# Kernel optimization log

Hardware: AMD Instinct MI355X
Metric: run time of the kernel (lower is better)

## Reference

```python
import jax, jax.numpy as jnp
import numpy as np

HIDDEN = 32


def setup_inputs() -> dict:
    key = jax.random.key(0)
    ks = jax.random.split(key, 7)
    B, T = 16384, 1024
    s = 1.0 / np.sqrt(HIDDEN)  # torch RNNCell/Linear init scale (uniform bound)
    return {
        "x": jax.random.normal(ks[0], (B, T, 1), dtype=jnp.float32),
        "W_ih": jax.random.uniform(ks[1], (HIDDEN, 1), jnp.float32, -s, s),
        "W_hh": jax.random.uniform(ks[2], (HIDDEN, HIDDEN), jnp.float32, -s, s),
        "b_ih": jax.random.uniform(ks[3], (HIDDEN,), jnp.float32, -s, s),
        "b_hh": jax.random.uniform(ks[4], (HIDDEN,), jnp.float32, -s, s),
        "fc_w": jax.random.uniform(ks[5], (1, HIDDEN), jnp.float32, -s, s),
        "fc_b": jax.random.uniform(ks[6], (1,), jnp.float32, -s, s),
    }


def reference(x, W_ih, W_hh, b_ih, b_hh, fc_w, fc_b):
    # x: [B, T, 1]; vanilla tanh RNN over T, then linear head on final hidden.
    B, T, _ = x.shape
    # Precompute input projections for all timesteps: [T, B, H]
    xi = jnp.einsum("bti,hi->tbh", x, W_ih) + b_ih + b_hh
    h0 = jnp.zeros((B, HIDDEN), dtype=x.dtype)

    def step(h, xi_t):
        h = jnp.tanh(xi_t + h @ W_hh.T)
        return h, None

    h_final, _ = jax.lax.scan(step, h0, xi)
    return h_final @ fc_w.T + fc_b  # [B, 1]
```

## Files before the change

kernel.cpp:

```cpp
#include <hip/hip_runtime.h>

#define T_LEN 1024

typedef _Float16 f16x8 __attribute__((ext_vector_type(8)));
typedef __fp16   fp16x2 __attribute__((ext_vector_type(2)));
typedef float    f32x4 __attribute__((ext_vector_type(4)));

__global__ __launch_bounds__(64) void rnn_fused(
    const float* __restrict__ x,
    const float* __restrict__ W_ih,
    const float* __restrict__ W_hh,
    const float* __restrict__ b_ih,
    const float* __restrict__ b_hh,
    const float* __restrict__ fc_w,
    const float* __restrict__ fc_b,
    float* __restrict__ out)
{
    const int lane = threadIdx.x;
    const int n = lane & 15;
    const int q = lane >> 4;

    const float K = 2.88539008177792681472f;

    const int c0row = 8 * (n >> 2) + (n & 3);
    const int c1row = c0row + 4;
    f16x8 a0, a1;
#pragma unroll
    for (int j = 0; j < 8; ++j) {
        a0[j] = (_Float16)(-2.0f * K * W_hh[c0row * 32 + q * 8 + j]);
        a1[j] = (_Float16)(-2.0f * K * W_hh[c1row * 32 + q * 8 + j]);
    }

    float wih[8], bias[8];
#pragma unroll
    for (int i = 0; i < 8; ++i) {
        int c = 8 * q + i;
        float rs = 0.0f;
        for (int k = 0; k < 32; ++k) rs += W_hh[c * 32 + k];
        wih[i]  = K * W_ih[c];
        bias[i] = K * (b_ih[c] + b_hh[c] + rs);
    }

    const float* xrow = x + (size_t)(blockIdx.x * 16 + n) * T_LEN;
    float4 xa = *(const float4*)xrow;

    f16x8 hb;
#pragma unroll
    for (int i = 0; i < 8; ++i) hb[i] = (_Float16)0.5f;

    for (int t4 = 0; t4 < T_LEN / 4; ++t4) {
        const int nt4 = (t4 < T_LEN / 4 - 1) ? t4 + 1 : t4;
        float4 xn = *(const float4*)(xrow + (size_t)nt4 * 4);
#pragma unroll
        for (int p = 0; p < 4; ++p) {
            const float xt = (p == 0) ? xa.x : (p == 1) ? xa.y : (p == 2) ? xa.z : xa.w;
            f32x4 acc0, acc1;
#pragma unroll
            for (int i = 0; i < 4; ++i) {
                acc0[i] = fmaf(xt, wih[i],     bias[i]);
                acc1[i] = fmaf(xt, wih[4 + i], bias[4 + i]);
            }
            acc0 = __builtin_amdgcn_mfma_f32_16x16x32_f16(a0, hb, acc0, 0, 0, 0);
            acc1 = __builtin_amdgcn_mfma_f32_16x16x32_f16(a1, hb, acc1, 0, 0, 0);

            float e0 = __builtin_amdgcn_exp2f(acc0[0]);
            float e1 = __builtin_amdgcn_exp2f(acc0[1]);
            float e2 = __builtin_amdgcn_exp2f(acc0[2]);
            float e3 = __builtin_amdgcn_exp2f(acc0[3]);
            float e4 = __builtin_amdgcn_exp2f(acc1[0]);
            float e5 = __builtin_amdgcn_exp2f(acc1[1]);
            float e6 = __builtin_amdgcn_exp2f(acc1[2]);
            float e7 = __builtin_amdgcn_exp2f(acc1[3]);
            float r0 = __builtin_amdgcn_rcpf(e0 + 1.0f);
            float r1 = __builtin_amdgcn_rcpf(e1 + 1.0f);
            float r2 = __builtin_amdgcn_rcpf(e2 + 1.0f);
            float r3 = __builtin_amdgcn_rcpf(e3 + 1.0f);
            float r4 = __builtin_amdgcn_rcpf(e4 + 1.0f);
            float r5 = __builtin_amdgcn_rcpf(e5 + 1.0f);
            float r6 = __builtin_amdgcn_rcpf(e6 + 1.0f);
            float r7 = __builtin_amdgcn_rcpf(e7 + 1.0f);

            struct H4 { fp16x2 p[4]; } hh;
            hh.p[0] = __builtin_amdgcn_cvt_pkrtz(r0, r1);
            hh.p[1] = __builtin_amdgcn_cvt_pkrtz(r2, r3);
            hh.p[2] = __builtin_amdgcn_cvt_pkrtz(r4, r5);
            hh.p[3] = __builtin_amdgcn_cvt_pkrtz(r6, r7);
            hb = __builtin_bit_cast(f16x8, hh);
        }
        xa = xn;
    }

    float part = 0.0f;
#pragma unroll
    for (int i = 0; i < 8; ++i) {
        float h = fmaf(-2.0f, (float)hb[i], 1.0f);
        part = fmaf(h, fc_w[8 * q + i], part);
    }
    part += __shfl_xor(part, 16);
    part += __shfl_xor(part, 32);
    if (q == 0) out[blockIdx.x * 16 + n] = part + fc_b[0];
}

extern "C" void kernel_launch(void* const* d_in, const int* in_sizes, int n_in,
                              void* d_out, int out_size, void* d_ws, size_t ws_size,
                              hipStream_t stream) {
    const float* x    = (const float*)d_in[0];
    const float* W_ih = (const float*)d_in[1];
    const float* W_hh = (const float*)d_in[2];
    const float* b_ih = (const float*)d_in[3];
    const float* b_hh = (const float*)d_in[4];
    const float* fc_w = (const float*)d_in[5];
    const float* fc_b = (const float*)d_in[6];
    float* out = (float*)d_out;

    const int B = in_sizes[0] / T_LEN;
    rnn_fused<<<B / 16, 64, 0, stream>>>(x, W_ih, W_hh, b_ih, b_hh, fc_w, fc_b, out);
}
```

Before: 254.9 us.

## Split hidden units across two wavefronts exchanging state through shared memory

Each 16-sequence block now runs two wavefronts, each computing 16 of the 32 hidden units with a single MFMA per step instead of two. The new hidden halves are written to a double-buffered LDS tile and read back after a block barrier to form the next step's input. This shortens each wave's serial chain of MFMA and transcendental work. In exchange it adds an LDS round trip and a __syncthreads on every one of the 1024 timesteps, which sits on the critical recurrence path.

```diff
diff --git a/kernel.cpp b/kernel.cpp
--- a/kernel.cpp
+++ b/kernel.cpp
@@ -6,7 +6,7 @@
 typedef __fp16   fp16x2 __attribute__((ext_vector_type(2)));
 typedef float    f32x4 __attribute__((ext_vector_type(4)));
 
-__global__ __launch_bounds__(64) void rnn_fused(
+__global__ __launch_bounds__(128) void rnn_fused(
     const float* __restrict__ x,
     const float* __restrict__ W_ih,
     const float* __restrict__ W_hh,
@@ -16,25 +16,25 @@
     const float* __restrict__ fc_b,
     float* __restrict__ out)
 {
-    const int lane = threadIdx.x;
+    const int tid  = threadIdx.x;
+    const int w    = tid >> 6;
+    const int lane = tid & 63;
     const int n = lane & 15;
     const int q = lane >> 4;
 
     const float K = 2.88539008177792681472f;
 
-    const int c0row = 8 * (n >> 2) + (n & 3);
-    const int c1row = c0row + 4;
-    f16x8 a0, a1;
+    __shared__ __align__(16) _Float16 rbuf[2][16][40];
+
+    f16x8 a;
 #pragma unroll
-    for (int j = 0; j < 8; ++j) {
-        a0[j] = (_Float16)(-2.0f * K * W_hh[c0row * 32 + q * 8 + j]);
-        a1[j] = (_Float16)(-2.0f * K * W_hh[c1row * 32 + q * 8 + j]);
-    }
+    for (int j = 0; j < 8; ++j)
+        a[j] = (_Float16)(-2.0f * K * W_hh[(16 * w + n) * 32 + 8 * q + j]);
 
-    float wih[8], bias[8];
+    float wih[4], bias[4];
 #pragma unroll
-    for (int i = 0; i < 8; ++i) {
-        int c = 8 * q + i;
+    for (int i = 0; i < 4; ++i) {
+        int c = 16 * w + 4 * q + i;
         float rs = 0.0f;
         for (int k = 0; k < 32; ++k) rs += W_hh[c * 32 + k];
         wih[i]  = K * W_ih[c];
@@ -48,57 +48,56 @@
 #pragma unroll
     for (int i = 0; i < 8; ++i) hb[i] = (_Float16)0.5f;
 
+    _Float16* wrp = &rbuf[0][n][16 * w + 4 * q];
+    const _Float16* rdp = &rbuf[0][n][8 * q];
+    const int BUFSTRIDE = 16 * 40;
+
     for (int t4 = 0; t4 < T_LEN / 4; ++t4) {
         const int nt4 = (t4 < T_LEN / 4 - 1) ? t4 + 1 : t4;
         float4 xn = *(const float4*)(xrow + (size_t)nt4 * 4);
 #pragma unroll
-        for (int p = 0; p < 4; ++p) {
-            const float xt = (p == 0) ? xa.x : (p == 1) ? xa.y : (p == 2) ? xa.z : xa.w;
-            f32x4 acc0, acc1;
+        for (int pp = 0; pp < 4; ++pp) {
+            const float xt = (pp == 0) ? xa.x : (pp == 1) ? xa.y : (pp == 2) ? xa.z : xa.w;
+            f32x4 acc;
 #pragma unroll
-            for (int i = 0; i < 4; ++i) {
-                acc0[i] = fmaf(xt, wih[i],     bias[i]);
-                acc1[i] = fmaf(xt, wih[4 + i], bias[4 + i]);
-            }
-            acc0 = __builtin_amdgcn_mfma_f32_16x16x32_f16(a0, hb, acc0, 0, 0, 0);
-            acc1 = __builtin_amdgcn_mfma_f32_16x16x32_f16(a1, hb, acc1, 0, 0, 0);
+            for (int i = 0; i < 4; ++i)
+                acc[i] = fmaf(xt, wih[i], bias[i]);
+            acc = __builtin_amdgcn_mfma_f32_16x16x32_f16(a, hb, acc, 0, 0, 0);
 
-            float e0 = __builtin_amdgcn_exp2f(acc0[0]);
-            float e1 = __builtin_amdgcn_exp2f(acc0[1]);
-            float e2 = __builtin_amdgcn_exp2f(acc0[2]);
-            float e3 = __builtin_amdgcn_exp2f(acc0[3]);
-            float e4 = __builtin_amdgcn_exp2f(acc1[0]);
-            float e5 = __builtin_amdgcn_exp2f(acc1[1]);
-            float e6 = __builtin_amdgcn_exp2f(acc1[2]);
-            float e7 = __builtin_amdgcn_exp2f(acc1[3]);
+            float e0 = __builtin_amdgcn_exp2f(acc[0]);
+            float e1 = __builtin_amdgcn_exp2f(acc[1]);
+            float e2 = __builtin_amdgcn_exp2f(acc[2]);
+            float e3 = __builtin_amdgcn_exp2f(acc[3]);
             float r0 = __builtin_amdgcn_rcpf(e0 + 1.0f);
             float r1 = __builtin_amdgcn_rcpf(e1 + 1.0f);
             float r2 = __builtin_amdgcn_rcpf(e2 + 1.0f);
             float r3 = __builtin_amdgcn_rcpf(e3 + 1.0f);
-            float r4 = __builtin_amdgcn_rcpf(e4 + 1.0f);
-            float r5 = __builtin_amdgcn_rcpf(e5 + 1.0f);
-            float r6 = __builtin_amdgcn_rcpf(e6 + 1.0f);
-            float r7 = __builtin_amdgcn_rcpf(e7 + 1.0f);
 
-            struct H4 { fp16x2 p[4]; } hh;
-            hh.p[0] = __builtin_amdgcn_cvt_pkrtz(r0, r1);
-            hh.p[1] = __builtin_amdgcn_cvt_pkrtz(r2, r3);
-            hh.p[2] = __builtin_amdgcn_cvt_pkrtz(r4, r5);
-            hh.p[3] = __builtin_amdgcn_cvt_pkrtz(r6, r7);
-            hb = __builtin_bit_cast(f16x8, hh);
+            struct H2 { fp16x2 a, b; } hh;
+            hh.a = __builtin_amdgcn_cvt_pkrtz(r0, r1);
+            hh.b = __builtin_amdgcn_cvt_pkrtz(r2, r3);
+            const unsigned long long wv =
+                __builtin_bit_cast(unsigned long long, hh);
+            *(unsigned long long*)(wrp + (pp & 1) * BUFSTRIDE) = wv;
+
+            __syncthreads();
+
+            hb = *(const f16x8*)(rdp + (pp & 1) * BUFSTRIDE);
         }
         xa = xn;
     }
 
-    float part = 0.0f;
+    if (w == 0) {
+        float part = 0.0f;
 #pragma unroll
-    for (int i = 0; i < 8; ++i) {
-        float h = fmaf(-2.0f, (float)hb[i], 1.0f);
-        part = fmaf(h, fc_w[8 * q + i], part);
+        for (int i = 0; i < 8; ++i) {
+            float h = fmaf(-2.0f, (float)hb[i], 1.0f);
+            part = fmaf(h, fc_w[8 * q + i], part);
+        }
+        part += __shfl_xor(part, 16);
+        part += __shfl_xor(part, 32);
+        if (q == 0) out[blockIdx.x * 16 + n] = part + fc_b[0];
     }
-    part += __shfl_xor(part, 16);
-    part += __shfl_xor(part, 32);
-    if (q == 0) out[blockIdx.x * 16 + n] = part + fc_b[0];
 }
 
 extern "C" void kernel_launch(void* const* d_in, const int* in_sizes, int n_in,
@@ -114,5 +113,5 @@
     float* out = (float*)d_out;
 
     const int B = in_sizes[0] / T_LEN;
-    rnn_fused<<<B / 16, 64, 0, stream>>>(x, W_ih, W_hh, b_ih, b_hh, fc_w, fc_b, out);
+    rnn_fused<<<B / 16, 128, 0, stream>>>(x, W_ih, W_hh, b_ih, b_hh, fc_w, fc_b, out);
 }
```

New measurement: 273.8 us. 7.4% more time.
